# Optimization experiments

Measured on AMD Instinct MI355X. Metric: run time of the kernel, lower is better.

## Reference

```python
import jax, jax.numpy as jnp
import numpy as np

BS, NA, HW, C, HEADS = 16, 256, 1024, 512, 8
FEAT_RES = 32  # hw = feat_res**2


def setup_inputs() -> dict:
    key = jax.random.key(0)
    ks = jax.random.split(key, 16)

    def lin_w(k, din, dout):
        return (jax.random.normal(k, (din, dout), jnp.float32) / np.sqrt(din)).astype(jnp.float32)

    inp = {
        "tok_agent": jax.random.normal(ks[0], (BS, NA, C), jnp.float32),
        "enc_feat_supp": jax.random.normal(ks[1], (BS, HW, C), jnp.float32),
        "enc_feat_query": jax.random.normal(ks[2], (BS, HW, C), jnp.float32),
        # projection weights stored as [in, out]
        "W_qa": lin_w(ks[3], C, C), "b_qa": jnp.zeros((C,), jnp.float32),
        "W_ks": lin_w(ks[4], C, C), "b_ks": jnp.zeros((C,), jnp.float32),
        "W_ka": lin_w(ks[5], C, C), "b_ka": jnp.zeros((C,), jnp.float32),
        "W_vs": lin_w(ks[6], C, C), "b_vs": jnp.zeros((C,), jnp.float32),
        # FFN: c -> 3c -> c
        "W_f1": lin_w(ks[7], C, 3 * C), "b_f1": jnp.zeros((3 * C,), jnp.float32),
        "W_f2": lin_w(ks[8], 3 * C, C), "b_f2": jnp.zeros((C,), jnp.float32),
    }
    return inp


def reference(tok_agent, enc_feat_supp, enc_feat_query,
              W_qa, b_qa, W_ks, b_ks, W_ka, b_ka, W_vs, b_vs,
              W_f1, b_f1, W_f2, b_f2):
    bs, na, c = tok_agent.shape
    hw = enc_feat_supp.shape[1]
    feat_res = int(round(np.sqrt(hw)))
    d_k_sqrt = np.float32(np.sqrt(c // HEADS))

    qa = tok_agent @ W_qa + b_qa                 # [bs, na, c]
    ks_ = enc_feat_supp @ W_ks + b_ks            # [bs, hw, c]
    qq = enc_feat_query @ W_qa + b_qa            # NOTE: original reuses qa_linear
    ka = tok_agent @ W_ka + b_ka                 # [bs, na, c]
    vs = enc_feat_supp @ W_vs + b_vs             # [bs, hw, c]

    scores_as = jnp.einsum('bac,bhc->bah', qa, ks_) / d_k_sqrt   # [bs, na, hw]
    scores_qa = jnp.einsum('bhc,bac->bha', qq, ka) / d_k_sqrt    # [bs, hw, na]

    # align_mat[b,i,j] = (argmax_a scores_as[b,a,i] == argmax_a scores_qa[b,j,a])
    a_idx = jnp.argmax(scores_as, axis=1)        # [bs, hw]
    b_idx = jnp.argmax(scores_qa, axis=2)        # [bs, hw]
    align = jnp.where(a_idx[:, :, None] == b_idx[:, None, :],
                      jnp.float32(0.0), jnp.float32(-1e6))       # [bs, hw, hw]

    # scores_sa @ scores_aq: [bs,hw,na] @ [bs,na,hw]
    logits = jnp.einsum('bai,bja->bij', scores_as, scores_qa)    # [bs, hw, hw]
    scores_qs = jax.nn.softmax(logits + align, axis=-1)

    # scores_qs^T @ vs : out[b,j,c] = sum_i scores_qs[b,i,j] * vs[b,i,c]
    dec = jnp.einsum('bij,bic->bjc', scores_qs, vs)              # [bs, hw, c]
    dec = jax.nn.relu(dec @ W_f1 + b_f1) @ W_f2 + b_f2           # FFN (dropout = eval identity)

    # raw memory reinterpretation, as in torch .view
    return dec.reshape(bs, c, feat_res, -1)
```

## Files before the change

kernel.cpp:

```cpp
#include <hip/hip_runtime.h>

typedef float          f32x4  __attribute__((ext_vector_type(4)));
typedef short          bf16x8 __attribute__((ext_vector_type(8)));
typedef _Float16       f16x8  __attribute__((ext_vector_type(8)));
typedef unsigned short u16x4  __attribute__((ext_vector_type(4)));

static constexpr int kBS = 16;
static constexpr int kHW = 1024;

__device__ __forceinline__ unsigned short f2bf(float x) {
  union { float f; unsigned int u; } v; v.f = x;
  unsigned int r = v.u + 0x7fffu + ((v.u >> 16) & 1u);
  return (unsigned short)(r >> 16);
}
__device__ __forceinline__ float bf2f(unsigned short h) {
  union { unsigned int u; float f; } v; v.u = ((unsigned int)h) << 16;
  return v.f;
}
__device__ __forceinline__ unsigned short h2u(_Float16 h) {
  union { _Float16 h; unsigned short u; } v; v.h = h; return v.u;
}

__device__ __forceinline__ void split2h(float x, unsigned short& u0, unsigned short& u1) {
  _Float16 h0 = (_Float16)x;
  if (fabsf(x) < 6.1035156e-05f) h0 = (_Float16)0.f;
  const float r = (x - (float)h0) * 4096.f;
  u0 = h2u(h0);
  u1 = h2u((_Float16)r);
}

__global__ __launch_bounds__(256)
void split_act2h(const f32x4* __restrict__ X, u16x4* __restrict__ P0,
                 u16x4* __restrict__ P1, int n4)
{
  int i = blockIdx.x * 256 + threadIdx.x;
  if (i >= n4) return;
  f32x4 x = X[i];
  u16x4 s0, s1;
#pragma unroll
  for (int u = 0; u < 4; ++u) {
    unsigned short a, b;
    split2h(x[u], a, b);
    s0[u] = a; s1[u] = b;
  }
  P0[i] = s0; P1[i] = s1;
}

__global__ __launch_bounds__(256)
void split_wT2h(const float* __restrict__ Wm, unsigned short* __restrict__ T0,
                unsigned short* __restrict__ T1, int K, int N)
{
  __shared__ float ts[32][33];
  const int k0 = blockIdx.x * 32, n0 = blockIdx.y * 32;
  const int tx = threadIdx.x, ty = threadIdx.y;
#pragma unroll
  for (int r = 0; r < 4; ++r)
    ts[ty + r * 8][tx] = Wm[(size_t)(k0 + ty + r * 8) * N + n0 + tx];
  __syncthreads();
#pragma unroll
  for (int r = 0; r < 4; ++r) {
    const int n = ty + r * 8;
    const size_t off = (size_t)(n0 + n) * K + k0 + tx;
    unsigned short a, b;
    split2h(ts[tx][n], a, b);
    T0[off] = a; T1[off] = b;
  }
}

template<bool F16>
__global__ __launch_bounds__(256)
void split_wT1(const float* __restrict__ Wm, unsigned short* __restrict__ T0,
               int K, int N)
{
  __shared__ float ts[32][33];
  const int k0 = blockIdx.x * 32, n0 = blockIdx.y * 32;
  const int tx = threadIdx.x, ty = threadIdx.y;
#pragma unroll
  for (int r = 0; r < 4; ++r)
    ts[ty + r * 8][tx] = Wm[(size_t)(k0 + ty + r * 8) * N + n0 + tx];
  __syncthreads();
#pragma unroll
  for (int r = 0; r < 4; ++r) {
    const int n = ty + r * 8;
    const float x = ts[tx][n];
    const size_t off = (size_t)(n0 + n) * K + k0 + tx;
    T0[off] = F16 ? h2u((_Float16)x) : f2bf(x);
  }
}

__device__ __forceinline__ void stage_tile(const unsigned short* src, int K,
                                           unsigned short* ldst, int wv, int lane)
{
#pragma unroll
  for (int i = 0; i < 2; ++i) {
    const int s   = wv * 128 + i * 64 + lane;
    const int row = s >> 2;
    const int gc  = ((s & 3) ^ ((row >> 1) & 3)) * 8;
    __builtin_amdgcn_global_load_lds(
        (const __attribute__((address_space(1))) void*)(src + (size_t)row * K + gc),
        (__attribute__((address_space(3))) void*)(ldst + ((wv * 128 + i * 64) << 3)),
        16, 0, 0);
  }
}

template<int ORD, int KU, int DEPTH, int OUTM, bool BIAS, bool RELU, bool F16IN>
__global__ __launch_bounds__(256)
void gke(const unsigned short* __restrict__ A0, const unsigned short* __restrict__ A1,
         const unsigned short* __restrict__ B0, const unsigned short* __restrict__ B1,
         const float* __restrict__ bias,
         float* __restrict__ Cf, unsigned short* __restrict__ O0,
         unsigned short* __restrict__ O1,
         int K, int ldc, long sA, long sB, long sC, long sBias, float scale)
{
  constexpr int NP   = ORD + 1;
  constexpr int NT   = 2 * NP;
  constexpr int TPP  = KU * NT;
  constexpr int LPP  = TPP * 2;
  static_assert(DEPTH == 2 || DEPTH == 4, "DEPTH in {2,4}");
  static_assert(LPP == 4 || LPP == 8 || LPP == 16, "vmcnt literals");
  extern __shared__ __align__(16) unsigned short lds[];

  const int tid  = threadIdx.x;
  const int wv   = tid >> 6, lane = tid & 63;
  const int wr   = wv >> 1,  wc   = wv & 1;
  const int cr   = lane & 15, cg  = lane >> 4;
  const int bm   = blockIdx.x * 128, bn = blockIdx.y * 128;

  const size_t zA = (size_t)blockIdx.z * (size_t)sA;
  const size_t zB = (size_t)blockIdx.z * (size_t)sB;
  const size_t zC = (size_t)blockIdx.z * (size_t)sC;
  const size_t zBias = (size_t)blockIdx.z * (size_t)sBias;

  const unsigned short* srcs[NT];
  srcs[0] = A0 + zA + (size_t)bm * K;
  if (NP == 2) srcs[1] = A1 + zA + (size_t)bm * K;
  srcs[NP + 0] = B0 + zB + (size_t)bn * K;
  if (NP == 2) srcs[NP + 1] = B1 + zB + (size_t)bn * K;

  f32x4 acc0[4][4], acc1[4][4];
#pragma unroll
  for (int i = 0; i < 4; ++i)
#pragma unroll
    for (int j = 0; j < 4; ++j)
#pragma unroll
      for (int r = 0; r < 4; ++r) {
        acc0[i][j][r] = 0.f;
        if (ORD == 1) acc1[i][j][r] = 0.f;
      }

#define STAGE_PH(ph, buf)                                                       \
  {                                                                             \
    _Pragma("unroll")                                                           \
    for (int u = 0; u < KU; ++u)                                                \
      _Pragma("unroll")                                                         \
      for (int t = 0; t < NT; ++t)                                              \
        stage_tile(srcs[t] + ((ph) * KU + u) * 32, K,                           \
                   lds + (size_t)((buf) * TPP + u * NT + t) * 4096, wv, lane);  \
  }
#define LOADA(u, pa)                                                            \
  {                                                                             \
    _Pragma("unroll")                                                           \
    for (int f = 0; f < 4; ++f) {                                               \
      const int ra = wr * 64 + f * 16 + cr;                                     \
      af[f] = *(const bf16x8*)&lb[(size_t)((u) * NT + (pa)) * 4096 +            \
                                  (ra * 4 + (cg ^ ((ra >> 1) & 3))) * 8];       \
    }                                                                           \
  }
#define DOPB(u, pb, ACC)                                                        \
  {                                                                             \
    bf16x8 bfr[4];                                                              \
    _Pragma("unroll")                                                           \
    for (int f = 0; f < 4; ++f) {                                               \
      const int rb = wc * 64 + f * 16 + cr;                                     \
      bfr[f] = *(const bf16x8*)&lb[(size_t)((u) * NT + NP + (pb)) * 4096 +      \
                                   (rb * 4 + (cg ^ ((rb >> 1) & 3))) * 8];      \
    }                                                                           \
    _Pragma("unroll")                                                           \
    for (int i = 0; i < 4; ++i)                                                 \
      _Pragma("unroll")                                                         \
      for (int j = 0; j < 4; ++j) {                                             \
        if constexpr (F16IN)                                                    \
          ACC[i][j] = __builtin_amdgcn_mfma_f32_16x16x32_f16(                   \
              __builtin_bit_cast(f16x8, af[i]), __builtin_bit_cast(f16x8, bfr[j]), \
              ACC[i][j], 0, 0, 0);                                              \
        else                                                                    \
          ACC[i][j] = __builtin_amdgcn_mfma_f32_16x16x32_bf16(af[i], bfr[j],    \
              ACC[i][j], 0, 0, 0);                                              \
      }                                                                         \
  }
#define COMPUTE_PH(buf)                                                         \
  {                                                                             \
    const unsigned short* lb = lds + (size_t)(buf) * TPP * 4096;                \
    bf16x8 af[4];                                                               \
    _Pragma("unroll")                                                           \
    for (int u = 0; u < KU; ++u) {                                              \
      if constexpr (ORD == 1) {                                                 \
        LOADA(u, 0); DOPB(u, 0, acc0); DOPB(u, 1, acc1);                        \
        LOADA(u, 1); DOPB(u, 0, acc1);                                          \
      } else {                                                                  \
        LOADA(u, 0); DOPB(u, 0, acc0);                                          \
      }                                                                         \
    }                                                                           \
  }

  const int nph = K / (32 * KU);
#pragma unroll
  for (int d = 0; d < DEPTH; ++d)
    if (d < nph) STAGE_PH(d, d);

  for (int ph = 0; ph < nph; ++ph) {
    const int rem = nph - 1 - ph;
    const int fut = rem < (DEPTH - 1) ? rem : (DEPTH - 1);
    if constexpr (LPP == 4) {
      if (fut >= 3)      asm volatile("s_waitcnt vmcnt(12)" ::: "memory");
      else if (fut == 2) asm volatile("s_waitcnt vmcnt(8)" ::: "memory");
      else if (fut == 1) asm volatile("s_waitcnt vmcnt(4)" ::: "memory");
      else               asm volatile("s_waitcnt vmcnt(0)" ::: "memory");
    } else if constexpr (LPP == 8) {
      if (fut >= 3)      asm volatile("s_waitcnt vmcnt(24)" ::: "memory");
      else if (fut == 2) asm volatile("s_waitcnt vmcnt(16)" ::: "memory");
      else if (fut == 1) asm volatile("s_waitcnt vmcnt(8)" ::: "memory");
      else               asm volatile("s_waitcnt vmcnt(0)" ::: "memory");
    } else {
      if (fut >= 1)      asm volatile("s_waitcnt vmcnt(16)" ::: "memory");
      else               asm volatile("s_waitcnt vmcnt(0)" ::: "memory");
    }
    __builtin_amdgcn_sched_barrier(0);
    __builtin_amdgcn_s_barrier();
    COMPUTE_PH(ph & (DEPTH - 1));
    __builtin_amdgcn_s_barrier();
    __builtin_amdgcn_sched_barrier(0);
    if (ph + DEPTH < nph) STAGE_PH(ph + DEPTH, ph & (DEPTH - 1));
  }
#undef STAGE_PH
#undef LOADA
#undef DOPB
#undef COMPUTE_PH

  const float RS = 2.44140625e-4f;
  float* CfB = Cf + zC;
  unsigned short* O0B = O0 + zC;
  unsigned short* O1B = O1 + zC;
#pragma unroll
  for (int fm = 0; fm < 4; ++fm) {
#pragma unroll
    for (int fn = 0; fn < 4; ++fn) {
      const int n  = bn + wc * 64 + fn * 16 + cr;
      const int m0 = bm + wr * 64 + fm * 16 + 4 * cg;
      float bv = 0.f;
      if (BIAS) bv = bias[zBias + n];
      if (OUTM == 4) {
        u16x4 o;
#pragma unroll
        for (int r = 0; r < 4; ++r) {
          float x = acc0[fm][fn][r];
          if constexpr (ORD == 1) x += acc1[fm][fn][r] * RS;
          x = x * scale + bv;
          if (RELU) x = fmaxf(x, 0.f);
          o[r] = f2bf(x);
        }
        *(u16x4*)(O0B + (size_t)n * ldc + m0) = o;
      } else {
#pragma unroll
        for (int r = 0; r < 4; ++r) {
          float x = acc0[fm][fn][r];
          if constexpr (ORD == 1) x += acc1[fm][fn][r] * RS;
          x = x * scale + bv;
          if (RELU) x = fmaxf(x, 0.f);
          const size_t off = (size_t)(m0 + r) * ldc + n;
          if (OUTM == 0) CfB[off] = x;
          else if (OUTM == 3) O0B[off] = f2bf(x);
          else {
            unsigned short a, b;
            split2h(x, a, b);
            O0B[off] = a; O1B[off] = b;
            if (OUTM == 2) CfB[off] = x;
          }
        }
      }
    }
  }
}

__global__ __launch_bounds__(256)
void row_argmax4(const float* __restrict__ X, int* __restrict__ out)
{
  const int row = blockIdx.x * 4 + (threadIdx.x >> 6);
  const float* xr = X + (size_t)row * 256;
  const int lane = threadIdx.x & 63;
  float best = -3.0e38f;
  int bi = 0;
#pragma unroll
  for (int t = 0; t < 4; ++t) {
    const int a = lane + (t << 6);
    const float x = xr[a];
    if (x > best) { best = x; bi = a; }
  }
#pragma unroll
  for (int off = 32; off >= 1; off >>= 1) {
    const float ov = __shfl_xor(best, off);
    const int   oi = __shfl_xor(bi, off);
    if (ov > best || (ov == best && oi < bi)) { best = ov; bi = oi; }
  }
  if (lane == 0) out[row] = bi;
}

__global__ __launch_bounds__(256)
void softmax_T(const float* __restrict__ Lg, const int* __restrict__ aidx,
               const int* __restrict__ bidx, unsigned short* __restrict__ PT,
               int ihalf)
{
  __shared__ int bj[1024];
  __shared__ unsigned short tile[1024 * 17];
  const int tid = threadIdx.x;
  const int i0  = blockIdx.x * 16;
  const int b   = blockIdx.y;
  const int r   = tid >> 4;
  const int l16 = tid & 15;

  for (int j = tid; j < 1024; j += 256) bj[j] = bidx[(b << 10) + j];
  __syncthreads();

  const int ai  = aidx[(b << 10) + (ihalf << 9) + i0 + r];
  const float* Lr = Lg + ((size_t)b * 512 + i0 + r) * 1024;
  const int jb = l16 * 64;

  float x[64];
  float mx = -3.0e38f;
#pragma unroll
  for (int q = 0; q < 16; ++q) {
    f32x4 f = *(const f32x4*)(Lr + jb + (q << 2));
#pragma unroll
    for (int u = 0; u < 4; ++u) {
      const int j = jb + (q << 2) + u;
      float t = f[u];
      if (bj[j] != ai) t -= 1e6f;
      x[(q << 2) + u] = t;
      mx = fmaxf(mx, t);
    }
  }
#pragma unroll
  for (int off = 8; off >= 1; off >>= 1) mx = fmaxf(mx, __shfl_xor(mx, off));
  float s = 0.f;
#pragma unroll
  for (int k = 0; k < 64; ++k) { float e = expf(x[k] - mx); x[k] = e; s += e; }
#pragma unroll
  for (int off = 8; off >= 1; off >>= 1) s += __shfl_xor(s, off);
  const float inv = 1.f / s;

#pragma unroll
  for (int k = 0; k < 64; ++k)
    tile[(jb + k) * 17 + r] = f2bf(x[k] * inv);
  __syncthreads();

  for (int j = tid; j < 1024; j += 256) {
    const unsigned short* tp = &tile[j * 17];
    unsigned int w[8];
#pragma unroll
    for (int q = 0; q < 8; ++q)
      w[q] = (unsigned int)tp[2 * q] | ((unsigned int)tp[2 * q + 1] << 16);
    const size_t off = ((size_t)b << 20) + ((size_t)j << 10) + (ihalf << 9) + i0;
    unsigned int* dst = (unsigned int*)(PT + off);
    *(uint4*)dst       = make_uint4(w[0], w[1], w[2], w[3]);
    *((uint4*)dst + 1) = make_uint4(w[4], w[5], w[6], w[7]);
  }
}

extern "C" void kernel_launch(void* const* d_in, const int* in_sizes, int n_in,
                              void* d_out, int out_size, void* d_ws, size_t ws_size,
                              hipStream_t stream)
{
  (void)in_sizes; (void)n_in; (void)out_size; (void)ws_size;

  const float* tok  = (const float*)d_in[0];
  const float* supp = (const float*)d_in[1];
  const float* qry  = (const float*)d_in[2];
  const float* W_qa = (const float*)d_in[3];
  const float* b_qa = (const float*)d_in[4];
  const float* W_ks = (const float*)d_in[5];
  const float* b_ks = (const float*)d_in[6];
  const float* W_ka = (const float*)d_in[7];
  const float* b_ka = (const float*)d_in[8];
  const float* W_vs = (const float*)d_in[9];
  const float* b_vs = (const float*)d_in[10];
  const float* W_f1 = (const float*)d_in[11];
  const float* b_f1 = (const float*)d_in[12];
  const float* W_f2 = (const float*)d_in[13];
  const float* b_f2 = (const float*)d_in[14];

  auto kProj  = &gke<1,1,2,1,true ,false,true >;
  auto kScore = &gke<1,2,2,2,false,false,true >;
  auto kLogit = &gke<1,1,2,0,false,false,true >;
  auto kVsT   = &gke<0,1,4,4,true ,false,true >;
  auto kPV    = &gke<0,1,4,3,false,false,false>;
  auto kFFN1  = &gke<0,1,4,3,true ,true ,false>;
  auto kFFN2  = &gke<0,1,4,0,true ,false,false>;
  hipFuncSetAttribute((const void*)kProj,  hipFuncAttributeMaxDynamicSharedMemorySize, 65536);
  hipFuncSetAttribute((const void*)kScore, hipFuncAttributeMaxDynamicSharedMemorySize, 131072);
  hipFuncSetAttribute((const void*)kLogit, hipFuncAttributeMaxDynamicSharedMemorySize, 65536);
  hipFuncSetAttribute((const void*)kVsT,   hipFuncAttributeMaxDynamicSharedMemorySize, 65536);
  hipFuncSetAttribute((const void*)kPV,    hipFuncAttributeMaxDynamicSharedMemorySize, 65536);
  hipFuncSetAttribute((const void*)kFFN1,  hipFuncAttributeMaxDynamicSharedMemorySize, 65536);
  hipFuncSetAttribute((const void*)kFFN2,  hipFuncAttributeMaxDynamicSharedMemorySize, 65536);

  char* W = (char*)d_ws;
  constexpr size_t MiB = 1048576;
  auto U = [&](double off) { return (unsigned short*)(W + (size_t)(off * MiB)); };
  auto F = [&](double off) { return (float*)(W + (size_t)(off * MiB)); };
  auto I = [&](double off) { return (int*)(W + (size_t)(off * MiB)); };

  const double oTOK0=0, oTOK1=4, oQTF=0, oSUP0=0, oSAF=0, oPT=0;
  const double oWQAT=16, oWKAT=17.5, oWKST=19, oWVST=20.5;
  const double oQA0=22, oQA1=26, oDEC=32, oKA0=34, oKA1=38;
  const double oQRY0=46, oQRY1=62, oQTP0=46, oQTP1=54;
  const double oSUP1=62, oVST=62, oSAP0=78, oSAP1=86;
  const double oQQ0=94, oQQ1=110, oLG=94, oMID=62;
  const double oWF1=142, oWF2=143.5, oBIA=148, oIDXB=150, oIDXA=150.0625;
  const double hP = 0.5;

  const dim3 B256(256), BW(32, 8);
  float* dummyF = F(oLG);
  unsigned short* dummyU = U(oLG);

  hipMemcpyAsync(W + (size_t)(oBIA * MiB), b_qa, 2048, hipMemcpyDeviceToDevice, stream);
  hipMemcpyAsync(W + (size_t)(oBIA * MiB) + 2048, b_ka, 2048, hipMemcpyDeviceToDevice, stream);

  split_wT2h<<<dim3(16,16), BW, 0, stream>>>(W_qa, U(oWQAT), U(oWQAT+hP), 512, 512);
  split_wT2h<<<dim3(16,16), BW, 0, stream>>>(W_ka, U(oWKAT), U(oWKAT+hP), 512, 512);
  split_wT2h<<<dim3(16,16), BW, 0, stream>>>(W_ks, U(oWKST), U(oWKST+hP), 512, 512);
  split_wT1<true><<<dim3(16,16), BW, 0, stream>>>(W_vs, U(oWVST), 512, 512);
  split_act2h<<<dim3(2048), B256, 0, stream>>>((const f32x4*)tok, (u16x4*)U(oTOK0), (u16x4*)U(oTOK1), 524288);
  kProj<<<dim3(32,4,2), B256, 65536, stream>>>(
      U(oTOK0),U(oTOK1), U(oWQAT),U(oWQAT+hP),
      F(oBIA), dummyF, U(oQA0),U(oQA1), 512, 512, 0, 786432, 6291456, 512, 1.f);
  split_act2h<<<dim3(8192), B256, 0, stream>>>((const f32x4*)qry, (u16x4*)U(oQRY0), (u16x4*)U(oQRY1), 2097152);
  kProj<<<dim3(128,4,1), B256, 65536, stream>>>(
      U(oQRY0),U(oQRY1), U(oWQAT),U(oWQAT+hP),
      b_qa, dummyF, U(oQQ0),U(oQQ1), 512, 512, 0,0,0,0, 1.f);
  kScore<<<dim3(8,2,16), B256, 131072, stream>>>(
      U(oQQ0),U(oQQ1), U(oKA0),U(oKA1),
      nullptr, F(oQTF), U(oQTP0),U(oQTP1), 512, 256,
      524288, 131072, 262144, 0, 0.125f);
  row_argmax4<<<dim3(kBS * kHW / 4), B256, 0, stream>>>(F(oQTF), I(oIDXB));
  split_act2h<<<dim3(8192), B256, 0, stream>>>((const f32x4*)supp, (u16x4*)U(oSUP0), (u16x4*)U(oSUP1), 2097152);
  kProj<<<dim3(128,4,1), B256, 65536, stream>>>(
      U(oSUP0),U(oSUP1), U(oWKST),U(oWKST+hP),
      b_ks, dummyF, U(oQQ0),U(oQQ1), 512, 512, 0,0,0,0, 1.f);
  kVsT<<<dim3(8,4,16), B256, 65536, stream>>>(
      U(oSUP0),dummyU, U(oWVST),dummyU,
      b_vs, dummyF, U(oVST),dummyU, 512, 1024,
      524288, 0, 524288, 0, 1.f);
  kScore<<<dim3(8,2,16), B256, 131072, stream>>>(
      U(oQQ0),U(oQQ1), U(oQA0),U(oQA1),
      nullptr, F(oSAF), U(oSAP0),U(oSAP1), 512, 256,
      524288, 131072, 262144, 0, 0.125f);
  row_argmax4<<<dim3(kBS * kHW / 4), B256, 0, stream>>>(F(oSAF), I(oIDXA));
  split_wT1<false><<<dim3(16,48), BW, 0, stream>>>(W_f1, U(oWF1), 512, 1536);
  split_wT1<false><<<dim3(48,16), BW, 0, stream>>>(W_f2, U(oWF2), 1536, 512);
  for (int h = 0; h < 2; ++h) {
    kLogit<<<dim3(4,8,16), B256, 65536, stream>>>(
        U(oSAP0) + (size_t)h*512*256, U(oSAP1) + (size_t)h*512*256,
        U(oQTP0), U(oQTP1),
        nullptr, F(oLG), dummyU,dummyU, 256, 1024,
        262144, 262144, 524288, 0, 1.f);
    softmax_T<<<dim3(32,16), B256, 0, stream>>>(F(oLG), I(oIDXA), I(oIDXB), U(oPT), h);
  }
  kPV<<<dim3(8,4,16), B256, 65536, stream>>>(
      U(oPT),dummyU, U(oVST),dummyU,
      nullptr, dummyF, U(oDEC),dummyU, 1024, 512,
      1048576, 524288, 524288, 0, 1.f);
  kFFN1<<<dim3(128,12,1), B256, 65536, stream>>>(
      U(oDEC),dummyU, U(oWF1),dummyU,
      b_f1, dummyF, U(oMID),dummyU, 512, 1536, 0,0,0,0, 1.f);
  kFFN2<<<dim3(128,4,1), B256, 65536, stream>>>(
      U(oMID),dummyU, U(oWF2),dummyU,
      b_f2, (float*)d_out, dummyU,dummyU, 1536, 512, 0,0,0,0, 1.f);
}
```

Baseline: 416.5 us.

## Add 256x256-tile 512-thread bf16 GEMM kernel for PV and FFN stages

Adds a new GEMM kernel with 256x256 output tiles, 8 waves and double-buffered LDS staging. It is used for the PV product and both FFN matmuls in place of the smaller-tile generic kernel, aiming for more operand reuse per LDS load and fewer global reads. It also drops the VsT projection pipeline depth from 4 to 2 with less LDS. The larger tiles produce fewer blocks (128 for PV and FFN2), which risks underfilling the GPU's CUs, and the 128 fp32 accumulators per thread raise register pressure.

```diff
diff --git a/kernel.cpp b/kernel.cpp
--- a/kernel.cpp
+++ b/kernel.cpp
@@ -100,6 +100,111 @@
         (const __attribute__((address_space(1))) void*)(src + (size_t)row * K + gc),
         (__attribute__((address_space(3))) void*)(ldst + ((wv * 128 + i * 64) << 3)),
         16, 0, 0);
+  }
+}
+
+__device__ __forceinline__ void stage_tile256(const unsigned short* src, int K,
+                                              unsigned short* ldst, int wv, int lane)
+{
+#pragma unroll
+  for (int i = 0; i < 2; ++i) {
+    const int s   = i * 512 + wv * 64 + lane;
+    const int row = s >> 2;
+    const int gc  = ((s & 3) ^ ((row >> 1) & 3)) * 8;
+    __builtin_amdgcn_global_load_lds(
+        (const __attribute__((address_space(1))) void*)(src + (size_t)row * K + gc),
+        (__attribute__((address_space(3))) void*)(ldst + ((i * 512 + wv * 64) << 3)),
+        16, 0, 0);
+  }
+}
+
+template<int OUTM, bool BIAS, bool RELU>
+__global__ __launch_bounds__(512)
+void gk256(const unsigned short* __restrict__ A0, const unsigned short* __restrict__ B0,
+           const float* __restrict__ bias,
+           float* __restrict__ Cf, unsigned short* __restrict__ O0,
+           int K, int ldc, long sA, long sB, long sC, float scale)
+{
+  extern __shared__ __align__(16) unsigned short lds[];
+
+  const int tid  = threadIdx.x;
+  const int wv   = tid >> 6, lane = tid & 63;
+  const int wr   = wv >> 2,  wc   = wv & 3;
+  const int cr   = lane & 15, cg  = lane >> 4;
+  const int bm   = blockIdx.x * 256, bn = blockIdx.y * 256;
+
+  const unsigned short* Ap = A0 + (size_t)blockIdx.z * (size_t)sA + (size_t)bm * K;
+  const unsigned short* Bp = B0 + (size_t)blockIdx.z * (size_t)sB + (size_t)bn * K;
+  const size_t zC = (size_t)blockIdx.z * (size_t)sC;
+
+  f32x4 acc[8][4];
+#pragma unroll
+  for (int i = 0; i < 8; ++i)
+#pragma unroll
+    for (int j = 0; j < 4; ++j)
+#pragma unroll
+      for (int r = 0; r < 4; ++r) acc[i][j][r] = 0.f;
+
+#define STAGE256(kt, buf)                                                      \
+  {                                                                            \
+    stage_tile256(Ap + (kt) * 32, K, lds + (size_t)(buf) * 16384,       wv, lane); \
+    stage_tile256(Bp + (kt) * 32, K, lds + (size_t)(buf) * 16384 + 8192, wv, lane); \
+  }
+
+  const int nt = K >> 5;
+  STAGE256(0, 0);
+  if (nt > 1) STAGE256(1, 1);
+
+  for (int kt = 0; kt < nt; ++kt) {
+    if (kt + 1 < nt) asm volatile("s_waitcnt vmcnt(4)" ::: "memory");
+    else             asm volatile("s_waitcnt vmcnt(0)" ::: "memory");
+    __builtin_amdgcn_sched_barrier(0);
+    __builtin_amdgcn_s_barrier();
+
+    const unsigned short* lb = lds + (size_t)(kt & 1) * 16384;
+    bf16x8 af[8], bf[4];
+#pragma unroll
+    for (int f = 0; f < 8; ++f) {
+      const int ra = wr * 128 + f * 16 + cr;
+      af[f] = *(const bf16x8*)&lb[(ra * 4 + (cg ^ ((ra >> 1) & 3))) * 8];
+    }
+#pragma unroll
+    for (int f = 0; f < 4; ++f) {
+      const int rb = wc * 64 + f * 16 + cr;
+      bf[f] = *(const bf16x8*)&lb[8192 + (rb * 4 + (cg ^ ((rb >> 1) & 3))) * 8];
+    }
+#pragma unroll
+    for (int i = 0; i < 8; ++i)
+#pragma unroll
+      for (int j = 0; j < 4; ++j)
+        acc[i][j] = __builtin_amdgcn_mfma_f32_16x16x32_bf16(af[i], bf[j], acc[i][j], 0, 0, 0);
+
+    __builtin_amdgcn_s_barrier();
+    __builtin_amdgcn_sched_barrier(0);
+    if (kt + 2 < nt) STAGE256(kt + 2, kt & 1);
+  }
+#undef STAGE256
+
+  float* CfB = Cf + zC;
+  unsigned short* O0B = O0 + zC;
+#pragma unroll
+  for (int fm = 0; fm < 8; ++fm) {
+#pragma unroll
+    for (int fn = 0; fn < 4; ++fn) {
+      const int n  = bn + wc * 64 + fn * 16 + cr;
+      const int m0 = bm + wr * 128 + fm * 16 + 4 * cg;
+      float bv = 0.f;
+      if (BIAS) bv = bias[n];
+      f32x4 v = acc[fm][fn];
+#pragma unroll
+      for (int r = 0; r < 4; ++r) {
+        float x = v[r] * scale + bv;
+        if (RELU) x = fmaxf(x, 0.f);
+        const size_t off = (size_t)(m0 + r) * ldc + n;
+        if (OUTM == 0) CfB[off] = x;
+        else O0B[off] = f2bf(x);
+      }
+    }
   }
 }
 
@@ -391,14 +496,14 @@
   auto kProj  = &gke<1,1,2,1,true ,false,true >;
   auto kScore = &gke<1,2,2,2,false,false,true >;
   auto kLogit = &gke<1,1,2,0,false,false,true >;
-  auto kVsT   = &gke<0,1,4,4,true ,false,true >;
-  auto kPV    = &gke<0,1,4,3,false,false,false>;
-  auto kFFN1  = &gke<0,1,4,3,true ,true ,false>;
-  auto kFFN2  = &gke<0,1,4,0,true ,false,false>;
+  auto kVsT   = &gke<0,1,2,4,true ,false,true >;
+  auto kPV    = &gk256<3,false,false>;
+  auto kFFN1  = &gk256<3,true ,true >;
+  auto kFFN2  = &gk256<0,true ,false>;
   hipFuncSetAttribute((const void*)kProj,  hipFuncAttributeMaxDynamicSharedMemorySize, 65536);
   hipFuncSetAttribute((const void*)kScore, hipFuncAttributeMaxDynamicSharedMemorySize, 131072);
   hipFuncSetAttribute((const void*)kLogit, hipFuncAttributeMaxDynamicSharedMemorySize, 65536);
-  hipFuncSetAttribute((const void*)kVsT,   hipFuncAttributeMaxDynamicSharedMemorySize, 65536);
+  hipFuncSetAttribute((const void*)kVsT,   hipFuncAttributeMaxDynamicSharedMemorySize, 32768);
   hipFuncSetAttribute((const void*)kPV,    hipFuncAttributeMaxDynamicSharedMemorySize, 65536);
   hipFuncSetAttribute((const void*)kFFN1,  hipFuncAttributeMaxDynamicSharedMemorySize, 65536);
   hipFuncSetAttribute((const void*)kFFN2,  hipFuncAttributeMaxDynamicSharedMemorySize, 65536);
@@ -418,7 +523,7 @@
   const double oWF1=142, oWF2=143.5, oBIA=148, oIDXB=150, oIDXA=150.0625;
   const double hP = 0.5;
 
-  const dim3 B256(256), BW(32, 8);
+  const dim3 B256(256), B512(512), BW(32, 8);
   float* dummyF = F(oLG);
   unsigned short* dummyU = U(oLG);
 
@@ -446,7 +551,7 @@
   kProj<<<dim3(128,4,1), B256, 65536, stream>>>(
       U(oSUP0),U(oSUP1), U(oWKST),U(oWKST+hP),
       b_ks, dummyF, U(oQQ0),U(oQQ1), 512, 512, 0,0,0,0, 1.f);
-  kVsT<<<dim3(8,4,16), B256, 65536, stream>>>(
+  kVsT<<<dim3(8,4,16), B256, 32768, stream>>>(
       U(oSUP0),dummyU, U(oWVST),dummyU,
       b_vs, dummyF, U(oVST),dummyU, 512, 1024,
       524288, 0, 524288, 0, 1.f);
@@ -465,14 +570,11 @@
         262144, 262144, 524288, 0, 1.f);
     softmax_T<<<dim3(32,16), B256, 0, stream>>>(F(oLG), I(oIDXA), I(oIDXB), U(oPT), h);
   }
-  kPV<<<dim3(8,4,16), B256, 65536, stream>>>(
-      U(oPT),dummyU, U(oVST),dummyU,
-      nullptr, dummyF, U(oDEC),dummyU, 1024, 512,
-      1048576, 524288, 524288, 0, 1.f);
-  kFFN1<<<dim3(128,12,1), B256, 65536, stream>>>(
-      U(oDEC),dummyU, U(oWF1),dummyU,
-      b_f1, dummyF, U(oMID),dummyU, 512, 1536, 0,0,0,0, 1.f);
-  kFFN2<<<dim3(128,4,1), B256, 65536, stream>>>(
-      U(oMID),dummyU, U(oWF2),dummyU,
-      b_f2, (float*)d_out, dummyU,dummyU, 1536, 512, 0,0,0,0, 1.f);
-}
+  kPV<<<dim3(4,2,16), B512, 65536, stream>>>(
+      U(oPT), U(oVST), nullptr, dummyF, U(oDEC), 1024, 512,
+      1048576, 524288, 524288, 1.f);
+  kFFN1<<<dim3(64,6,1), B512, 65536, stream>>>(
+      U(oDEC), U(oWF1), b_f1, dummyF, U(oMID), 512, 1536, 0,0,0, 1.f);
+  kFFN2<<<dim3(64,2,1), B512, 65536, stream>>>(
+      U(oMID), U(oWF2), b_f2, (float*)d_out, dummyU, 1536, 512, 0,0,0, 1.f);
+}
```

After: 424.6 us. Within noise of the previous version (+1.9%).

## Fuse row argmax into score GEMM epilogue via packed atomicMax keys

Applied to the files above, without the earlier changes.

Adds an epilogue mode to the score GEMM that reduces each row to a packed 64-bit key (monotone float bits plus inverted column index) and merges it globally with atomicMax. This replaces the separate fp32 score write and the two row_argmax kernels, and softmax decodes the indices from the keys. It also lowers the pipeline depth of the V projection, PV and FFN GEMMs from 4 to 2, which halves their shared memory and may allow more blocks per CU. The costs are two memsets, the atomics and a shallower prefetch pipeline. Ties still resolve to the lowest index, matching argmax.

```diff
diff --git a/kernel.cpp b/kernel.cpp
--- a/kernel.cpp
+++ b/kernel.cpp
@@ -19,6 +19,10 @@
 }
 __device__ __forceinline__ unsigned short h2u(_Float16 h) {
   union { _Float16 h; unsigned short u; } v; v.h = h; return v.u;
+}
+__device__ __forceinline__ unsigned int fmono(float f) {
+  union { float f; unsigned int u; } v; v.f = f;
+  return (v.u & 0x80000000u) ? ~v.u : (v.u | 0x80000000u);
 }
 
 __device__ __forceinline__ void split2h(float x, unsigned short& u0, unsigned short& u1) {
@@ -109,7 +113,7 @@
          const unsigned short* __restrict__ B0, const unsigned short* __restrict__ B1,
          const float* __restrict__ bias,
          float* __restrict__ Cf, unsigned short* __restrict__ O0,
-         unsigned short* __restrict__ O1,
+         unsigned short* __restrict__ O1, unsigned long long* __restrict__ keys,
          int K, int ldc, long sA, long sB, long sC, long sBias, float scale)
 {
   constexpr int NP   = ORD + 1;
@@ -241,6 +245,43 @@
   float* CfB = Cf + zC;
   unsigned short* O0B = O0 + zC;
   unsigned short* O1B = O1 + zC;
+
+  if constexpr (OUTM == 5) {
+#pragma unroll
+    for (int fm = 0; fm < 4; ++fm) {
+      const int m0 = bm + wr * 64 + fm * 16 + 4 * cg;
+      unsigned long long bk[4] = {0ull, 0ull, 0ull, 0ull};
+#pragma unroll
+      for (int fn = 0; fn < 4; ++fn) {
+        const int n = bn + wc * 64 + fn * 16 + cr;
+#pragma unroll
+        for (int r = 0; r < 4; ++r) {
+          const float x = (acc0[fm][fn][r] + acc1[fm][fn][r] * RS) * scale;
+          unsigned short a, b;
+          split2h(x, a, b);
+          const size_t off = (size_t)(m0 + r) * ldc + n;
+          O0B[off] = a; O1B[off] = b;
+          const unsigned long long k =
+              ((unsigned long long)fmono(x) << 32) | (unsigned)(255 - n);
+          if (k > bk[r]) bk[r] = k;
+        }
+      }
+#pragma unroll
+      for (int r = 0; r < 4; ++r) {
+        unsigned long long k = bk[r];
+#pragma unroll
+        for (int o = 1; o < 16; o <<= 1) {
+          const unsigned long long ok =
+              (unsigned long long)__shfl_xor((long long)k, o, 16);
+          if (ok > k) k = ok;
+        }
+        if ((lane & 15) == 0)
+          atomicMax(keys + (size_t)blockIdx.z * 1024 + (m0 + r), k);
+      }
+    }
+    return;
+  }
+
 #pragma unroll
   for (int fm = 0; fm < 4; ++fm) {
 #pragma unroll
@@ -283,32 +324,9 @@
 }
 
 __global__ __launch_bounds__(256)
-void row_argmax4(const float* __restrict__ X, int* __restrict__ out)
-{
-  const int row = blockIdx.x * 4 + (threadIdx.x >> 6);
-  const float* xr = X + (size_t)row * 256;
-  const int lane = threadIdx.x & 63;
-  float best = -3.0e38f;
-  int bi = 0;
-#pragma unroll
-  for (int t = 0; t < 4; ++t) {
-    const int a = lane + (t << 6);
-    const float x = xr[a];
-    if (x > best) { best = x; bi = a; }
-  }
-#pragma unroll
-  for (int off = 32; off >= 1; off >>= 1) {
-    const float ov = __shfl_xor(best, off);
-    const int   oi = __shfl_xor(bi, off);
-    if (ov > best || (ov == best && oi < bi)) { best = ov; bi = oi; }
-  }
-  if (lane == 0) out[row] = bi;
-}
-
-__global__ __launch_bounds__(256)
-void softmax_T(const float* __restrict__ Lg, const int* __restrict__ aidx,
-               const int* __restrict__ bidx, unsigned short* __restrict__ PT,
-               int ihalf)
+void softmax_T(const float* __restrict__ Lg, const unsigned long long* __restrict__ keysA,
+               const unsigned long long* __restrict__ keysB,
+               unsigned short* __restrict__ PT, int ihalf)
 {
   __shared__ int bj[1024];
   __shared__ unsigned short tile[1024 * 17];
@@ -318,10 +336,11 @@
   const int r   = tid >> 4;
   const int l16 = tid & 15;
 
-  for (int j = tid; j < 1024; j += 256) bj[j] = bidx[(b << 10) + j];
+  for (int j = tid; j < 1024; j += 256)
+    bj[j] = 255 - (int)(keysB[(b << 10) + j] & 0xFFFFFFFFull);
   __syncthreads();
 
-  const int ai  = aidx[(b << 10) + (ihalf << 9) + i0 + r];
+  const int ai = 255 - (int)(keysA[(b << 10) + (ihalf << 9) + i0 + r] & 0xFFFFFFFFull);
   const float* Lr = Lg + ((size_t)b * 512 + i0 + r) * 1024;
   const int jb = l16 * 64;
 
@@ -389,41 +408,44 @@
   const float* b_f2 = (const float*)d_in[14];
 
   auto kProj  = &gke<1,1,2,1,true ,false,true >;
-  auto kScore = &gke<1,2,2,2,false,false,true >;
+  auto kScore = &gke<1,2,2,5,false,false,true >;
   auto kLogit = &gke<1,1,2,0,false,false,true >;
-  auto kVsT   = &gke<0,1,4,4,true ,false,true >;
-  auto kPV    = &gke<0,1,4,3,false,false,false>;
-  auto kFFN1  = &gke<0,1,4,3,true ,true ,false>;
-  auto kFFN2  = &gke<0,1,4,0,true ,false,false>;
+  auto kVsT   = &gke<0,1,2,4,true ,false,true >;
+  auto kPV    = &gke<0,1,2,3,false,false,false>;
+  auto kFFN1  = &gke<0,1,2,3,true ,true ,false>;
+  auto kFFN2  = &gke<0,1,2,0,true ,false,false>;
   hipFuncSetAttribute((const void*)kProj,  hipFuncAttributeMaxDynamicSharedMemorySize, 65536);
   hipFuncSetAttribute((const void*)kScore, hipFuncAttributeMaxDynamicSharedMemorySize, 131072);
   hipFuncSetAttribute((const void*)kLogit, hipFuncAttributeMaxDynamicSharedMemorySize, 65536);
-  hipFuncSetAttribute((const void*)kVsT,   hipFuncAttributeMaxDynamicSharedMemorySize, 65536);
-  hipFuncSetAttribute((const void*)kPV,    hipFuncAttributeMaxDynamicSharedMemorySize, 65536);
-  hipFuncSetAttribute((const void*)kFFN1,  hipFuncAttributeMaxDynamicSharedMemorySize, 65536);
-  hipFuncSetAttribute((const void*)kFFN2,  hipFuncAttributeMaxDynamicSharedMemorySize, 65536);
+  hipFuncSetAttribute((const void*)kVsT,   hipFuncAttributeMaxDynamicSharedMemorySize, 32768);
+  hipFuncSetAttribute((const void*)kPV,    hipFuncAttributeMaxDynamicSharedMemorySize, 32768);
+  hipFuncSetAttribute((const void*)kFFN1,  hipFuncAttributeMaxDynamicSharedMemorySize, 32768);
+  hipFuncSetAttribute((const void*)kFFN2,  hipFuncAttributeMaxDynamicSharedMemorySize, 32768);
 
   char* W = (char*)d_ws;
   constexpr size_t MiB = 1048576;
   auto U = [&](double off) { return (unsigned short*)(W + (size_t)(off * MiB)); };
   auto F = [&](double off) { return (float*)(W + (size_t)(off * MiB)); };
-  auto I = [&](double off) { return (int*)(W + (size_t)(off * MiB)); };
-
-  const double oTOK0=0, oTOK1=4, oQTF=0, oSUP0=0, oSAF=0, oPT=0;
+  auto KY = [&](double off) { return (unsigned long long*)(W + (size_t)(off * MiB)); };
+
+  const double oTOK0=0, oTOK1=4, oSUP0=0, oPT=0;
   const double oWQAT=16, oWKAT=17.5, oWKST=19, oWVST=20.5;
   const double oQA0=22, oQA1=26, oDEC=32, oKA0=34, oKA1=38;
   const double oQRY0=46, oQRY1=62, oQTP0=46, oQTP1=54;
   const double oSUP1=62, oVST=62, oSAP0=78, oSAP1=86;
   const double oQQ0=94, oQQ1=110, oLG=94, oMID=62;
-  const double oWF1=142, oWF2=143.5, oBIA=148, oIDXB=150, oIDXA=150.0625;
+  const double oWF1=142, oWF2=143.5, oBIA=148, oKEYB=148.5, oKEYA=148.75;
   const double hP = 0.5;
 
   const dim3 B256(256), BW(32, 8);
   float* dummyF = F(oLG);
   unsigned short* dummyU = U(oLG);
+  unsigned long long* dummyK = KY(oLG);
 
   hipMemcpyAsync(W + (size_t)(oBIA * MiB), b_qa, 2048, hipMemcpyDeviceToDevice, stream);
   hipMemcpyAsync(W + (size_t)(oBIA * MiB) + 2048, b_ka, 2048, hipMemcpyDeviceToDevice, stream);
+  hipMemsetAsync(KY(oKEYB), 0, kBS * kHW * 8, stream);
+  hipMemsetAsync(KY(oKEYA), 0, kBS * kHW * 8, stream);
 
   split_wT2h<<<dim3(16,16), BW, 0, stream>>>(W_qa, U(oWQAT), U(oWQAT+hP), 512, 512);
   split_wT2h<<<dim3(16,16), BW, 0, stream>>>(W_ka, U(oWKAT), U(oWKAT+hP), 512, 512);
@@ -432,47 +454,45 @@
   split_act2h<<<dim3(2048), B256, 0, stream>>>((const f32x4*)tok, (u16x4*)U(oTOK0), (u16x4*)U(oTOK1), 524288);
   kProj<<<dim3(32,4,2), B256, 65536, stream>>>(
       U(oTOK0),U(oTOK1), U(oWQAT),U(oWQAT+hP),
-      F(oBIA), dummyF, U(oQA0),U(oQA1), 512, 512, 0, 786432, 6291456, 512, 1.f);
+      F(oBIA), dummyF, U(oQA0),U(oQA1), dummyK, 512, 512, 0, 786432, 6291456, 512, 1.f);
   split_act2h<<<dim3(8192), B256, 0, stream>>>((const f32x4*)qry, (u16x4*)U(oQRY0), (u16x4*)U(oQRY1), 2097152);
   kProj<<<dim3(128,4,1), B256, 65536, stream>>>(
       U(oQRY0),U(oQRY1), U(oWQAT),U(oWQAT+hP),
-      b_qa, dummyF, U(oQQ0),U(oQQ1), 512, 512, 0,0,0,0, 1.f);
+      b_qa, dummyF, U(oQQ0),U(oQQ1), dummyK, 512, 512, 0,0,0,0, 1.f);
   kScore<<<dim3(8,2,16), B256, 131072, stream>>>(
       U(oQQ0),U(oQQ1), U(oKA0),U(oKA1),
-      nullptr, F(oQTF), U(oQTP0),U(oQTP1), 512, 256,
+      nullptr, dummyF, U(oQTP0),U(oQTP1), KY(oKEYB), 512, 256,
       524288, 131072, 262144, 0, 0.125f);
-  row_argmax4<<<dim3(kBS * kHW / 4), B256, 0, stream>>>(F(oQTF), I(oIDXB));
   split_act2h<<<dim3(8192), B256, 0, stream>>>((const f32x4*)supp, (u16x4*)U(oSUP0), (u16x4*)U(oSUP1), 2097152);
   kProj<<<dim3(128,4,1), B256, 65536, stream>>>(
       U(oSUP0),U(oSUP1), U(oWKST),U(oWKST+hP),
-      b_ks, dummyF, U(oQQ0),U(oQQ1), 512, 512, 0,0,0,0, 1.f);
-  kVsT<<<dim3(8,4,16), B256, 65536, stream>>>(
+      b_ks, dummyF, U(oQQ0),U(oQQ1), dummyK, 512, 512, 0,0,0,0, 1.f);
+  kVsT<<<dim3(8,4,16), B256, 32768, stream>>>(
       U(oSUP0),dummyU, U(oWVST),dummyU,
-      b_vs, dummyF, U(oVST),dummyU, 512, 1024,
+      b_vs, dummyF, U(oVST),dummyU, dummyK, 512, 1024,
       524288, 0, 524288, 0, 1.f);
   kScore<<<dim3(8,2,16), B256, 131072, stream>>>(
       U(oQQ0),U(oQQ1), U(oQA0),U(oQA1),
-      nullptr, F(oSAF), U(oSAP0),U(oSAP1), 512, 256,
+      nullptr, dummyF, U(oSAP0),U(oSAP1), KY(oKEYA), 512, 256,
       524288, 131072, 262144, 0, 0.125f);
-  row_argmax4<<<dim3(kBS * kHW / 4), B256, 0, stream>>>(F(oSAF), I(oIDXA));
   split_wT1<false><<<dim3(16,48), BW, 0, stream>>>(W_f1, U(oWF1), 512, 1536);
   split_wT1<false><<<dim3(48,16), BW, 0, stream>>>(W_f2, U(oWF2), 1536, 512);
   for (int h = 0; h < 2; ++h) {
     kLogit<<<dim3(4,8,16), B256, 65536, stream>>>(
         U(oSAP0) + (size_t)h*512*256, U(oSAP1) + (size_t)h*512*256,
         U(oQTP0), U(oQTP1),
-        nullptr, F(oLG), dummyU,dummyU, 256, 1024,
+        nullptr, F(oLG), dummyU,dummyU, dummyK, 256, 1024,
         262144, 262144, 524288, 0, 1.f);
-    softmax_T<<<dim3(32,16), B256, 0, stream>>>(F(oLG), I(oIDXA), I(oIDXB), U(oPT), h);
-  }
-  kPV<<<dim3(8,4,16), B256, 65536, stream>>>(
+    softmax_T<<<dim3(32,16), B256, 0, stream>>>(F(oLG), KY(oKEYA), KY(oKEYB), U(oPT), h);
+  }
+  kPV<<<dim3(8,4,16), B256, 32768, stream>>>(
       U(oPT),dummyU, U(oVST),dummyU,
-      nullptr, dummyF, U(oDEC),dummyU, 1024, 512,
+      nullptr, dummyF, U(oDEC),dummyU, dummyK, 1024, 512,
       1048576, 524288, 524288, 0, 1.f);
-  kFFN1<<<dim3(128,12,1), B256, 65536, stream>>>(
+  kFFN1<<<dim3(128,12,1), B256, 32768, stream>>>(
       U(oDEC),dummyU, U(oWF1),dummyU,
-      b_f1, dummyF, U(oMID),dummyU, 512, 1536, 0,0,0,0, 1.f);
-  kFFN2<<<dim3(128,4,1), B256, 65536, stream>>>(
+      b_f1, dummyF, U(oMID),dummyU, dummyK, 512, 1536, 0,0,0,0, 1.f);
+  kFFN2<<<dim3(128,4,1), B256, 32768, stream>>>(
       U(oMID),dummyU, U(oWF2),dummyU,
-      b_f2, (float*)d_out, dummyU,dummyU, 1536, 512, 0,0,0,0, 1.f);
-}
+      b_f2, (float*)d_out, dummyU,dummyU, dummyK, 1536, 512, 0,0,0,0, 1.f);
+}
```

Result: faster. 407.1 us (-2.3%).
